# Optimization experiments

Measured on AMD Instinct MI355X. Metric: run time of the kernel, lower is better.

## Reference

```python
import jax, jax.numpy as jnp
import numpy as np
import math

D_MODEL = 512
N_HEADS = 8
D_FF = 2048
E_LAYERS = 2
ENC_IN = 3
MA_K = 25            # moving_avg kernel size
FACTOR = 1
B, L_CYC, CDL = 16, 20, 128
SEQ = L_CYC * CDL    # 2560
TOP_K = int(FACTOR * math.log(SEQ))  # 7
OUTPUT_NUM = 1


def moving_avg(x, k=MA_K):
    # x: [B,S,D]; replicate-pad ends by (k-1)//2, stride-1 mean pool -> length S
    p = (k - 1) // 2
    xp = jnp.concatenate([jnp.repeat(x[:, :1], p, axis=1), x, jnp.repeat(x[:, -1:], p, axis=1)], axis=1)
    c = jnp.cumsum(xp, axis=1)
    c = jnp.concatenate([jnp.zeros_like(c[:, :1]), c], axis=1)
    return (c[:, k:] - c[:, :-k]) / k


def token_embed(x, W):
    # x: [B,S,C], W: [D_MODEL, C, 3]; Conv1d k=3, circular padding, no bias
    xc = jnp.pad(x.transpose(0, 2, 1), ((0, 0), (0, 0), (1, 1)), mode='wrap')
    y = jax.lax.conv_general_dilated(xc, W, (1,), 'VALID', dimension_numbers=('NCH', 'OIH', 'NCH'))
    return y.transpose(0, 2, 1)  # [B,S,D]


def autocorrelation(q, k, v):
    # q,k,v: [B,S,H,E]; FFT autocorrelation + top-k time-delay aggregation (inference path)
    B_, S, H, E = q.shape
    qf = jnp.fft.rfft(q.transpose(0, 2, 3, 1), axis=-1)      # [B,H,E,F]
    kf = jnp.fft.rfft(k.transpose(0, 2, 3, 1), axis=-1)
    corr = jnp.fft.irfft(qf * jnp.conj(kf), n=S, axis=-1)    # [B,H,E,S]
    vals = v.transpose(0, 2, 3, 1)                           # [B,H,E,S]
    mean_corr = corr.mean(axis=(1, 2))                       # [B,S]
    weights, delay = jax.lax.top_k(mean_corr, TOP_K)         # [B,K]
    w = jax.nn.softmax(weights, axis=-1)

    def agg_one(v_b, d_b, w_b):
        # roll by -delay == gather values at index (t + delay) mod S
        out = jnp.zeros_like(v_b)
        for i in range(TOP_K):
            out = out + jnp.roll(v_b, -d_b[i], axis=-1) * w_b[i]
        return out

    V = jax.vmap(agg_one)(vals, delay, w)                    # [B,H,E,S]
    return V.transpose(0, 3, 1, 2)                           # [B,S,H,E]


def my_layernorm(x, g, b):
    # LayerNorm over last dim, then subtract the per-series (time) mean
    mu = x.mean(-1, keepdims=True)
    var = ((x - mu) ** 2).mean(-1, keepdims=True)
    xh = (x - mu) / jnp.sqrt(var + 1e-5) * g + b
    return xh - xh.mean(axis=1, keepdims=True)


def encoder_layer(x, Wq, bq, Wk, bk, Wv, bv, Wo, bo, Wc1, Wc2):
    B_, S, D = x.shape
    H, E = N_HEADS, D // N_HEADS
    q = (x @ Wq + bq).reshape(B_, S, H, E)
    k = (x @ Wk + bk).reshape(B_, S, H, E)
    v = (x @ Wv + bv).reshape(B_, S, H, E)
    att = autocorrelation(q, k, v).reshape(B_, S, D)
    x = x + (att @ Wo + bo)
    x = x - moving_avg(x)                                    # series_decomp1: residual part
    y = jax.nn.gelu(x @ Wc1, approximate=False) @ Wc2        # 1x1 convs, no bias
    z = x + y
    return z - moving_avg(z)                                 # series_decomp2


def setup_inputs() -> dict:
    key = jax.random.key(0)
    ks = jax.random.split(key, 12)
    s = 0.02
    rn = lambda k, shape: jax.random.normal(k, shape, dtype=jnp.float32) * s
    return {
        'cycle_curve_data': jax.random.normal(ks[0], (B, L_CYC, ENC_IN, CDL), dtype=jnp.float32),
        'curve_attn_mask': jnp.ones((B, L_CYC), dtype=jnp.float32),
        'W_emb': rn(ks[1], (D_MODEL, ENC_IN, 3)),
        'Wq': rn(ks[2], (E_LAYERS, D_MODEL, D_MODEL)),
        'bq': jnp.zeros((E_LAYERS, D_MODEL), jnp.float32),
        'Wk': rn(ks[3], (E_LAYERS, D_MODEL, D_MODEL)),
        'bk': jnp.zeros((E_LAYERS, D_MODEL), jnp.float32),
        'Wv': rn(ks[4], (E_LAYERS, D_MODEL, D_MODEL)),
        'bv': jnp.zeros((E_LAYERS, D_MODEL), jnp.float32),
        'Wo': rn(ks[5], (E_LAYERS, D_MODEL, D_MODEL)),
        'bo': jnp.zeros((E_LAYERS, D_MODEL), jnp.float32),
        'Wc1': rn(ks[6], (E_LAYERS, D_MODEL, D_FF)),
        'Wc2': rn(ks[7], (E_LAYERS, D_FF, D_MODEL)),
        'gamma': jnp.ones((D_MODEL,), jnp.float32),
        'beta': jnp.zeros((D_MODEL,), jnp.float32),
        'Wp': rn(ks[8], (D_MODEL * SEQ, OUTPUT_NUM)),
        'bp': jnp.zeros((OUTPUT_NUM,), jnp.float32),
    }


def reference(cycle_curve_data, curve_attn_mask, W_emb, Wq, bq, Wk, bk, Wv, bv, Wo, bo, Wc1, Wc2, gamma, beta, Wp, bp):
    mask = curve_attn_mask[:, :, None, None]                 # [B,L,1,1]
    x = jnp.where(mask == 0, 0.0, cycle_curve_data)          # zero masked cycles
    Bn = x.shape[0]
    x = x.transpose(0, 1, 3, 2).reshape(Bn, SEQ, ENC_IN)     # [B, L*CDL, NV]
    h = token_embed(x, W_emb)                                # DataEmbedding_wo_pos (x_mark=None, dropout=0)
    for l in range(E_LAYERS):
        h = encoder_layer(h, Wq[l], bq[l], Wk[l], bk[l], Wv[l], bv[l], Wo[l], bo[l], Wc1[l], Wc2[l])
    h = my_layernorm(h, gamma, beta)
    out = jax.nn.gelu(h, approximate=False)
    emb = out.reshape(Bn, -1)
    return emb @ Wp + bp                                     # [B, OUTPUT_NUM]
```

## Files before the change

kernel.cpp:

```cpp
#include <hip/hip_runtime.h>
#include <math.h>

#define BATCH 16
#define L_CYC 20
#define CDL 128
#define SEQ 2560
#define ENC_IN 3
#define DMODEL 512
#define DFF 2048
#define NLAYERS 2
#define TOPK 7
#define MROWS (BATCH*SEQ)
#define SD ((size_t)BATCH * SEQ * DMODEL)
#define FFN_CHUNK 20480
#define CHUNK_D 256
#define DGRP 8
#define FFT_NT 512

typedef short bf16x8 __attribute__((ext_vector_type(8)));
typedef float f32x4 __attribute__((ext_vector_type(4)));

__device__ __forceinline__ float gelu_f(float x) {
    return 0.5f * x * (1.0f + erff(x * 0.70710678118654752f));
}
__device__ __forceinline__ unsigned short f2bf(float f) {
    unsigned int u = __float_as_uint(f);
    u += 0x7fff + ((u >> 16) & 1);
    return (unsigned short)(u >> 16);
}
__device__ __forceinline__ float bf2f(unsigned short h) {
    return __uint_as_float(((unsigned int)h) << 16);
}
__device__ __forceinline__ void xcd_map(int p, int G, int& g, int& n) {
    int a = p >> 3;
    n = a % G;
    g = (a / G) * 8 + (p & 7);
}
__device__ __forceinline__ void gload16(const unsigned short* g, unsigned short* l) {
    typedef unsigned int u32;
    __builtin_amdgcn_global_load_lds(
        (const __attribute__((address_space(1))) u32*)g,
        (__attribute__((address_space(3))) u32*)l, 16, 0, 0);
}

__global__ __launch_bounds__(256) void embed_kernel(
    const float* __restrict__ data, const float* __restrict__ mask,
    const float* __restrict__ Wemb, float* __restrict__ h) {
    __shared__ float xv[9];
    size_t idx = (size_t)blockIdx.x * 256 + threadIdx.x;
    size_t r = idx >> 9;
    int s = (int)(r % SEQ);
    int b = (int)(r / SEQ);
    int tid = threadIdx.x;
    if (tid < 9) {
        int t = tid / 3, c = tid % 3;
        int u = s - 1 + t;
        if (u < 0) u += SEQ;
        if (u >= SEQ) u -= SEQ;
        int cyc = u >> 7, pos = u & 127;
        float mk = mask[b * L_CYC + cyc];
        xv[c * 3 + t] = (mk == 0.f) ? 0.f
            : data[(((size_t)b * L_CYC + cyc) * ENC_IN + c) * CDL + pos];
    }
    __syncthreads();
    int dm = idx & (DMODEL - 1);
    float acc = 0.f;
#pragma unroll
    for (int j = 0; j < 9; j++) acc += xv[j] * Wemb[dm * 9 + j];
    h[idx] = acc;
}

__global__ void conv_split_kernel(const float* __restrict__ in,
                                  unsigned short* __restrict__ hi,
                                  unsigned short* __restrict__ lo, size_t n) {
    size_t i = ((size_t)blockIdx.x * 256 + threadIdx.x) * 4;
    if (i >= n) return;
    float4 v = *(const float4*)(in + i);
    float vv[4] = { v.x, v.y, v.z, v.w };
#pragma unroll
    for (int j = 0; j < 4; j++) {
        unsigned short h = f2bf(vv[j]);
        hi[i + j] = h;
        lo[i + j] = f2bf(vv[j] - bf2f(h));
    }
}

__global__ __launch_bounds__(256) void transpose_bf16_kernel(
    const float* __restrict__ W, unsigned short* __restrict__ Wt, int K, int N) {
    __shared__ float t[32][33];
    int n0 = blockIdx.x * 32, k0 = blockIdx.y * 32;
    int c = threadIdx.x & 31, r = threadIdx.x >> 5;
    for (int i = 0; i < 4; i++)
        t[r + i * 8][c] = W[(size_t)(k0 + r + i * 8) * N + n0 + c];
    __syncthreads();
    for (int i = 0; i < 4; i++)
        Wt[(size_t)(n0 + r + i * 8) * K + k0 + c] = f2bf(t[c][r + i * 8]);
}

__global__ __launch_bounds__(256) void transpose_split_stk_kernel(
    const float* __restrict__ W, unsigned short* __restrict__ WtH,
    unsigned short* __restrict__ WtL, int which) {
    __shared__ float t[32][33];
    int n0 = blockIdx.x * 32, k0 = blockIdx.y * 32;
    int c = threadIdx.x & 31, r = threadIdx.x >> 5;
    for (int i = 0; i < 4; i++)
        t[r + i * 8][c] = W[(size_t)(k0 + r + i * 8) * DMODEL + n0 + c];
    __syncthreads();
    for (int i = 0; i < 4; i++) {
        int n = n0 + r + i * 8;
        int row = (n & 255) + ((n >> 8) * 512) + which * 256;
        float v = t[c][r + i * 8];
        unsigned short h = f2bf(v);
        size_t o = (size_t)row * DMODEL + k0 + c;
        WtH[o] = h;
        WtL[o] = f2bf(v - bf2f(h));
    }
}

__global__ void stack_bias_kernel(const float* __restrict__ bq,
                                  const float* __restrict__ bk, float* __restrict__ bstk) {
    int i = blockIdx.x * 256 + threadIdx.x;
    if (i >= 1024) return;
    int c = i >> 9, j = i & 511;
    bstk[i] = (j < 256) ? bq[c * 256 + j] : bk[c * 256 + (j - 256)];
}

__global__ __launch_bounds__(256) void wvo_kernel(
    const float* __restrict__ Wv, const float* __restrict__ Wo,
    float* __restrict__ Wvo) {
    __shared__ float row[DMODEL];
    int k = blockIdx.x;
    int tid = threadIdx.x;
    for (int j = tid; j < DMODEL; j += 256) row[j] = Wv[(size_t)k * DMODEL + j];
    __syncthreads();
    float a0 = 0.f, a1 = 0.f;
    for (int j = 0; j < DMODEL; j++) {
        float wv = row[j];
        a0 += wv * Wo[(size_t)j * DMODEL + tid];
        a1 += wv * Wo[(size_t)j * DMODEL + tid + 256];
    }
    Wvo[(size_t)k * DMODEL + tid] = a0;
    Wvo[(size_t)k * DMODEL + tid + 256] = a1;
}

__global__ void cbias_kernel(const float* __restrict__ bv, const float* __restrict__ Wo,
                             const float* __restrict__ bo, float* __restrict__ cb) {
    int n = blockIdx.x * 256 + threadIdx.x;
    if (n >= DMODEL) return;
    float acc = bo[n];
    for (int j = 0; j < DMODEL; j++) acc += bv[j] * Wo[(size_t)j * DMODEL + n];
    cb[n] = acc;
}

#define BK 32
__global__ __launch_bounds__(256) void gemm_mfma_kernel(
    const unsigned short* __restrict__ A, const unsigned short* __restrict__ Wt,
    const float* __restrict__ bias, const float* res,
    void* Cout, int M, int N, int K, int act, int outMode, int gridN)
{
    __shared__ unsigned short As[128 * 32];
    __shared__ unsigned short Bs[128 * 32];
    int tid = threadIdx.x;
    int wave = tid >> 6, lane = tid & 63;
    int wm = wave & 1, wn = wave >> 1;
    int gblk, nblk;
    xcd_map(blockIdx.x, gridN, gblk, nblk);
    int bm = gblk * 128, bn = nblk * 128;

    int lrs = lane >> 2;
    int lk  = (lane & 3) * 8;

    f32x4 acc[4][4] = {};
    int frow = lane & 15, fk = (lane >> 4) * 8;

    for (int k0 = 0; k0 < K; k0 += BK) {
        __syncthreads();
#pragma unroll
        for (int i = 0; i < 2; i++) {
            int j = wave * 2 + i;
            int row = j * 16 + lrs;
            gload16(A  + (size_t)(bm + row) * K + k0 + lk, As + j * 512);
            gload16(Wt + (size_t)(bn + row) * K + k0 + lk, Bs + j * 512);
        }
        asm volatile("s_waitcnt vmcnt(0)" ::: "memory");
        __syncthreads();
        bf16x8 af[4], bfv[4];
#pragma unroll
        for (int mi = 0; mi < 4; mi++)
            af[mi] = *(const bf16x8*)&As[(wm * 64 + mi * 16 + frow) * 32 + fk];
#pragma unroll
        for (int nj = 0; nj < 4; nj++)
            bfv[nj] = *(const bf16x8*)&Bs[(wn * 64 + nj * 16 + frow) * 32 + fk];
#pragma unroll
        for (int mi = 0; mi < 4; mi++)
#pragma unroll
            for (int nj = 0; nj < 4; nj++)
                acc[mi][nj] = __builtin_amdgcn_mfma_f32_16x16x32_bf16(
                    af[mi], bfv[nj], acc[mi][nj], 0, 0, 0);
    }

    int lrow = (lane >> 4) * 4, lcol = lane & 15;
#pragma unroll
    for (int mi = 0; mi < 4; mi++) {
        int row0 = bm + wm * 64 + mi * 16 + lrow;
#pragma unroll
        for (int nj = 0; nj < 4; nj++) {
            int col = bn + wn * 64 + nj * 16 + lcol;
            float bv = bias ? bias[col] : 0.f;
            f32x4 v = acc[mi][nj];
#pragma unroll
            for (int r = 0; r < 4; r++) {
                int row = row0 + r;
                float x = v[r] + bv;
                if (res) x += res[(size_t)row * N + col];
                if (act == 1) x = gelu_f(x);
                if (outMode == 0) ((float*)Cout)[(size_t)row * N + col] = x;
                else              ((unsigned short*)Cout)[(size_t)row * N + col] = f2bf(x);
            }
        }
    }
}

__global__ __launch_bounds__(256) void gemm_qk_split_kernel(
    const unsigned short* __restrict__ Ahi, const unsigned short* __restrict__ Alo,
    const unsigned short* __restrict__ Whi, const unsigned short* __restrict__ Wlo,
    const float* __restrict__ bias, float* __restrict__ Ct, int M, int K, int gridN)
{
    __shared__ unsigned short AsH[128 * 32];
    __shared__ unsigned short AsL[128 * 32];
    __shared__ unsigned short BsH[128 * 32];
    __shared__ unsigned short BsL[128 * 32];
    int tid = threadIdx.x;
    int wave = tid >> 6, lane = tid & 63;
    int wm = wave & 1, wn = wave >> 1;
    int gblk, nblk;
    xcd_map(blockIdx.x, gridN, gblk, nblk);
    int bm = gblk * 128, bn = nblk * 128;

    int lrs = lane >> 2;
    int lk  = (lane & 3) * 8;

    f32x4 acc[4][4] = {};
    int frow = lane & 15, fk = (lane >> 4) * 8;

    for (int k0 = 0; k0 < K; k0 += BK) {
        __syncthreads();
#pragma unroll
        for (int i = 0; i < 2; i++) {
            int j = wave * 2 + i;
            int row = j * 16 + lrs;
            size_t oa = (size_t)(bm + row) * K + k0 + lk;
            size_t ob = (size_t)(bn + row) * K + k0 + lk;
            gload16(Ahi + oa, AsH + j * 512);
            gload16(Alo + oa, AsL + j * 512);
            gload16(Whi + ob, BsH + j * 512);
            gload16(Wlo + ob, BsL + j * 512);
        }
        asm volatile("s_waitcnt vmcnt(0)" ::: "memory");
        __syncthreads();
        bf16x8 afh[4], afl[4], bfh[4], bfl[4];
#pragma unroll
        for (int mi = 0; mi < 4; mi++) {
            int o = (wm * 64 + mi * 16 + frow) * 32 + fk;
            afh[mi] = *(const bf16x8*)&AsH[o];
            afl[mi] = *(const bf16x8*)&AsL[o];
        }
#pragma unroll
        for (int nj = 0; nj < 4; nj++) {
            int o = (wn * 64 + nj * 16 + frow) * 32 + fk;
            bfh[nj] = *(const bf16x8*)&BsH[o];
            bfl[nj] = *(const bf16x8*)&BsL[o];
        }
#pragma unroll
        for (int mi = 0; mi < 4; mi++)
#pragma unroll
            for (int nj = 0; nj < 4; nj++) {
                acc[mi][nj] = __builtin_amdgcn_mfma_f32_16x16x32_bf16(
                    afh[mi], bfh[nj], acc[mi][nj], 0, 0, 0);
                acc[mi][nj] = __builtin_amdgcn_mfma_f32_16x16x32_bf16(
                    afh[mi], bfl[nj], acc[mi][nj], 0, 0, 0);
                acc[mi][nj] = __builtin_amdgcn_mfma_f32_16x16x32_bf16(
                    afl[mi], bfh[nj], acc[mi][nj], 0, 0, 0);
            }
    }

    int lrow = (lane >> 4) * 4, lcol = lane & 15;
#pragma unroll
    for (int mi = 0; mi < 4; mi++) {
        int row0 = bm + wm * 64 + mi * 16 + lrow;
#pragma unroll
        for (int nj = 0; nj < 4; nj++) {
            int col = bn + wn * 64 + nj * 16 + lcol;
            float bv = bias ? bias[col] : 0.f;
            f32x4 v = acc[mi][nj];
#pragma unroll
            for (int r = 0; r < 4; r++)
                Ct[(size_t)col * M + row0 + r] = v[r] + bv;
        }
    }
}

__device__ __forceinline__ int swz(int a) { return a ^ ((a >> 4) & 15); }

template<int LOGS, int NT>
__device__ __forceinline__ void radix4_stage(const float2* __restrict__ X,
                                             float2* __restrict__ Y,
                                             const float2* __restrict__ w512x,
                                             int tid) {
    const int s = 1 << LOGS;
    for (int t = tid; t < 640; t += NT) {
        int sub = t >> 7, r = t & 127;
        int base = sub << 9;
        int q = r & (s - 1);
        int ps = r - q;
        float2 x0 = X[swz(base + r)];
        float2 x1 = X[swz(base + r + 128)];
        float2 x2 = X[swz(base + r + 256)];
        float2 x3 = X[swz(base + r + 384)];
        float A0r = x0.x + x2.x, A0i = x0.y + x2.y;
        float B0r = x1.x + x3.x, B0i = x1.y + x3.y;
        float A1r = x0.x - x2.x, A1i = x0.y - x2.y;
        float B1r = x1.x - x3.x, B1i = x1.y - x3.y;
        float2 w1 = w512x[ps];
        float w2r = w1.x * w1.x - w1.y * w1.y;
        float w2i = 2.0f * w1.x * w1.y;
        float w3r = w2r * w1.x - w2i * w1.y;
        float w3i = w2r * w1.y + w2i * w1.x;
        float u1r = A1r + B1i, u1i = A1i - B1r;
        float u2r = A0r - B0r, u2i = A0i - B0i;
        float u3r = A1r - B1i, u3i = A1i + B1r;
        int ob = base + q + 4 * ps;
        Y[swz(ob)]         = make_float2(A0r + B0r, A0i + B0i);
        Y[swz(ob + s)]     = make_float2(u1r * w1.x - u1i * w1.y,
                                         u1r * w1.y + u1i * w1.x);
        Y[swz(ob + 2 * s)] = make_float2(u2r * w2r - u2i * w2i,
                                         u2r * w2i + u2i * w2r);
        Y[swz(ob + 3 * s)] = make_float2(u3r * w3r - u3i * w3i,
                                         u3r * w3i + u3i * w3r);
    }
}

template<int NT>
__device__ void fft2560(float2* bufA, float2* bufB, const float2* w512x,
                        const float2* tw, int tid) {
    __syncthreads();
    {
        const float w5r[5] = { 1.f,  0.30901699437494742f, -0.80901699437494742f,
                              -0.80901699437494742f,  0.30901699437494742f };
        const float w5i[5] = { 0.f, -0.95105651629515357f, -0.58778525229247312f,
                               0.58778525229247312f,  0.95105651629515357f };
        float2 x[5];
#pragma unroll
        for (int n1 = 0; n1 < 5; n1++) x[n1] = bufA[swz(n1 * 512 + tid)];
#pragma unroll
        for (int k1 = 0; k1 < 5; k1++) {
            float ar = 0.f, ai = 0.f;
#pragma unroll
            for (int n1 = 0; n1 < 5; n1++) {
                int m = (n1 * k1) % 5;
                ar += x[n1].x * w5r[m] - x[n1].y * w5i[m];
                ai += x[n1].x * w5i[m] + x[n1].y * w5r[m];
            }
            if (k1 == 0) {
                bufB[swz(tid)] = make_float2(ar, ai);
            } else {
                float2 w = tw[k1 - 1];
                bufB[swz(k1 * 512 + tid)] =
                    make_float2(ar * w.x - ai * w.y, ar * w.y + ai * w.x);
            }
        }
    }
    __syncthreads();
    radix4_stage<0, NT>(bufB, bufA, w512x, tid); __syncthreads();
    radix4_stage<2, NT>(bufA, bufB, w512x, tid); __syncthreads();
    radix4_stage<4, NT>(bufB, bufA, w512x, tid); __syncthreads();
    radix4_stage<6, NT>(bufA, bufB, w512x, tid); __syncthreads();
    for (int t = tid; t < 1280; t += NT) {
        int sub = t >> 8, q = t & 255;
        int base = sub << 9;
        float2 a = bufB[swz(base + q)];
        float2 b = bufB[swz(base + q + 256)];
        bufA[swz(base + q)]       = make_float2(a.x + b.x, a.y + b.y);
        bufA[swz(base + q + 256)] = make_float2(a.x - b.x, a.y - b.y);
    }
    __syncthreads();
}

__global__ __launch_bounds__(FFT_NT) void fft_fwd_kernel(
    const float* __restrict__ qt, const float* __restrict__ kt, float* __restrict__ Z)
{
    __shared__ float2 bufA[SEQ];
    __shared__ float2 bufB[SEQ];
    __shared__ float2 w512x[512];
    int d0 = blockIdx.x * DGRP;
    int b = blockIdx.y;
    int tid = threadIdx.x;
    {
        float sn, cs;
        sincosf(-6.283185307179586f * (float)tid / 512.0f, &sn, &cs);
        w512x[tid] = make_float2(cs, sn);
    }
    float2 tw[4];
#pragma unroll
    for (int k1 = 1; k1 <= 4; k1++) {
        float sn, cs;
        sincosf(-2.4543692606170259e-3f * (float)(k1 * tid), &sn, &cs);
        tw[k1 - 1] = make_float2(cs, sn);
    }
    float accR[5], accI[5];
#pragma unroll
    for (int j = 0; j < 5; j++) { accR[j] = 0.f; accI[j] = 0.f; }

    for (int col = 0; col < DGRP; col++) {
        const float* qcol = qt + (size_t)(d0 + col) * MROWS + (size_t)b * SEQ;
        const float* kcol = kt + (size_t)(d0 + col) * MROWS + (size_t)b * SEQ;
        __syncthreads();
        for (int i = tid; i < SEQ; i += FFT_NT)
            bufA[swz(i)] = make_float2(qcol[i], kcol[i]);
        fft2560<FFT_NT>(bufA, bufB, w512x, tw, tid);
#pragma unroll
        for (int j = 0; j < 5; j++) {
            int f = tid + FFT_NT * j;
            int fpos = (f % 5) * 512 + (f / 5);
            int g = f ? (SEQ - f) : 0;
            int gpos = (g % 5) * 512 + (g / 5);
            float2 Z1 = bufA[swz(fpos)], Z2 = bufA[swz(gpos)];
            accR[j] += 0.5f * (Z1.x * Z2.y + Z1.y * Z2.x);
            accI[j] += 0.25f * ((Z1.x * Z1.x + Z1.y * Z1.y)
                              - (Z2.x * Z2.x + Z2.y * Z2.y));
        }
    }
#pragma unroll
    for (int j = 0; j < 5; j++) {
        int f = tid + FFT_NT * j;
        int fpos = (f % 5) * 512 + (f / 5);
        atomicAdd(&Z[((size_t)b * SEQ + fpos) * 2 + 0], accR[j]);
        atomicAdd(&Z[((size_t)b * SEQ + fpos) * 2 + 1], accI[j]);
    }
}

__global__ __launch_bounds__(FFT_NT) void fft_inv_kernel(
    const float* __restrict__ Z, float* __restrict__ mc)
{
    __shared__ float2 bufA[SEQ];
    __shared__ float2 bufB[SEQ];
    __shared__ float2 w512x[512];
    int b = blockIdx.x;
    int tid = threadIdx.x;
    {
        float sn, cs;
        sincosf(-6.283185307179586f * (float)tid / 512.0f, &sn, &cs);
        w512x[tid] = make_float2(cs, sn);
    }
    float2 tw[4];
#pragma unroll
    for (int k1 = 1; k1 <= 4; k1++) {
        float sn, cs;
        sincosf(-2.4543692606170259e-3f * (float)(k1 * tid), &sn, &cs);
        tw[k1 - 1] = make_float2(cs, sn);
    }
    for (int i = tid; i < SEQ; i += FFT_NT) {
        int k1 = i % 5, k2 = i / 5;
        float zr = Z[((size_t)b * SEQ + k1 * 512 + k2) * 2 + 0];
        float zi = Z[((size_t)b * SEQ + k1 * 512 + k2) * 2 + 1];
        bufA[swz(i)] = make_float2(zr, -zi);
    }
    fft2560<FFT_NT>(bufA, bufB, w512x, tw, tid);
    const float scale = 1.0f / (2560.0f * 512.0f);
    for (int j = tid; j < SEQ; j += FFT_NT) {
        int k1 = j >> 9, k2 = j & 511;
        mc[(size_t)b * SEQ + k1 + 5 * k2] = bufA[swz(j)].x * scale;
    }
}

__global__ __launch_bounds__(256) void topk_kernel(
    const float* __restrict__ mc, float* __restrict__ wts, int* __restrict__ dels)
{
    __shared__ float cv[SEQ];
    __shared__ float rv[256];
    __shared__ int   ri[256];
    __shared__ float topv[TOPK];
    __shared__ int   topi[TOPK];
    int b = blockIdx.x, tid = threadIdx.x;
    for (int i = tid; i < SEQ; i += 256) cv[i] = mc[(size_t)b * SEQ + i];
    __syncthreads();
    for (int it = 0; it < TOPK; it++) {
        float bv = -2e30f; int bi = 1 << 30;
        for (int i = tid; i < SEQ; i += 256) {
            float v = cv[i];
            if (v > bv || (v == bv && i < bi)) { bv = v; bi = i; }
        }
        rv[tid] = bv; ri[tid] = bi;
        __syncthreads();
        for (int off = 128; off > 0; off >>= 1) {
            if (tid < off) {
                float v2 = rv[tid + off]; int i2 = ri[tid + off];
                if (v2 > rv[tid] || (v2 == rv[tid] && i2 < ri[tid])) {
                    rv[tid] = v2; ri[tid] = i2;
                }
            }
            __syncthreads();
        }
        if (tid == 0) { topv[it] = rv[0]; topi[it] = ri[0]; cv[ri[0]] = -1e30f; }
        __syncthreads();
    }
    if (tid == 0) {
        float mx = topv[0];
        float e[TOPK], ssum = 0.f;
        for (int i = 0; i < TOPK; i++) { e[i] = expf(topv[i] - mx); ssum += e[i]; }
        for (int i = 0; i < TOPK; i++) {
            wts[b * TOPK + i] = e[i] / ssum;
            dels[b * TOPK + i] = topi[i];
        }
    }
}

__global__ void agg_res_kernel(const float* __restrict__ u, const float* __restrict__ x,
                               const float* __restrict__ cb,
                               const float* __restrict__ wts, const int* __restrict__ dels,
                               float* __restrict__ x1) {
    size_t idx = (size_t)blockIdx.x * 256 + threadIdx.x;
    if (idx >= SD) return;
    int d = idx & (DMODEL - 1);
    size_t r = idx >> 9;
    int s = (int)(r % SEQ);
    int b = (int)(r / SEQ);
    float acc = cb[d] + x[idx];
    for (int i = 0; i < TOPK; i++) {
        int del = dels[b * TOPK + i];
        float w = wts[b * TOPK + i];
        int ss = s + del; if (ss >= SEQ) ss -= SEQ;
        acc += w * u[((size_t)b * SEQ + ss) * DMODEL + d];
    }
    x1[idx] = acc;
}

#define MA_MODE_PLAIN 0
#define MA_MODE_BF    1
#define MA_MODE_SPLIT 2
template<int MODE>
__device__ __forceinline__ void ma_run_body(
    const float* __restrict__ x, float* __restrict__ out,
    unsigned short* __restrict__ o1, unsigned short* __restrict__ o2)
{
    int tid = threadIdx.x;
    int s0 = blockIdx.x * 128;
    int d  = blockIdx.y * 256 + tid;
    int b  = blockIdx.z;
    const float* xb = x + (size_t)b * SEQ * DMODEL + d;
    float sum = 0.f;
#pragma unroll
    for (int j = -12; j <= 12; j++) {
        int ss = s0 + j;
        ss = ss < 0 ? 0 : (ss > SEQ - 1 ? SEQ - 1 : ss);
        sum += xb[(size_t)ss * DMODEL];
    }
    for (int s = s0; s < s0 + 128; s++) {
        float v = xb[(size_t)s * DMODEL] - sum * (1.0f / 25.0f);
        size_t o = ((size_t)b * SEQ + s) * DMODEL + d;
        out[o] = v;
        if (MODE == MA_MODE_BF) {
            o1[o] = f2bf(v);
        } else if (MODE == MA_MODE_SPLIT) {
            unsigned short h = f2bf(v);
            o1[o] = h;
            o2[o] = f2bf(v - bf2f(h));
        }
        int add = s + 13; if (add > SEQ - 1) add = SEQ - 1;
        int sub = s - 12; if (sub < 0) sub = 0;
        sum += xb[(size_t)add * DMODEL] - xb[(size_t)sub * DMODEL];
    }
}
__global__ __launch_bounds__(256) void ma_sub_kernel(
    const float* __restrict__ x, float* __restrict__ out) {
    ma_run_body<MA_MODE_PLAIN>(x, out, nullptr, nullptr);
}
__global__ __launch_bounds__(256) void ma_sub_bf_kernel(
    const float* __restrict__ x, float* __restrict__ out,
    unsigned short* __restrict__ obf) {
    ma_run_body<MA_MODE_BF>(x, out, obf, nullptr);
}
__global__ __launch_bounds__(256) void ma_sub_split_kernel(
    const float* __restrict__ x, float* __restrict__ out,
    unsigned short* __restrict__ hi, unsigned short* __restrict__ lo) {
    ma_run_body<MA_MODE_SPLIT>(x, out, hi, lo);
}

__global__ __launch_bounds__(256) void ln_kernel(
    const float* __restrict__ x, const float* __restrict__ g,
    const float* __restrict__ be, float* __restrict__ xh)
{
    int row = blockIdx.x;
    int tid = threadIdx.x;
    __shared__ float red[256];
    const float* xr = x + (size_t)row * DMODEL;
    float v0 = xr[tid], v1 = xr[tid + 256];
    red[tid] = v0 + v1;
    __syncthreads();
    for (int off = 128; off > 0; off >>= 1) {
        if (tid < off) red[tid] += red[tid + off];
        __syncthreads();
    }
    float mu = red[0] / (float)DMODEL;
    __syncthreads();
    float d0 = v0 - mu, d1 = v1 - mu;
    red[tid] = d0 * d0 + d1 * d1;
    __syncthreads();
    for (int off = 128; off > 0; off >>= 1) {
        if (tid < off) red[tid] += red[tid + off];
        __syncthreads();
    }
    float inv = rsqrtf(red[0] / (float)DMODEL + 1e-5f);
    xh[(size_t)row * DMODEL + tid]       = d0 * inv * g[tid] + be[tid];
    xh[(size_t)row * DMODEL + tid + 256] = d1 * inv * g[tid + 256] + be[tid + 256];
}

__global__ __launch_bounds__(256) void colmean_kernel(
    const float* __restrict__ xh, float* __restrict__ cm) {
    int idx = blockIdx.x * 256 + threadIdx.x;
    int d = idx & (DMODEL - 1), b = idx >> 9;
    int s0 = blockIdx.y * 128;
    float acc = 0.f;
    for (int s = s0; s < s0 + 128; s++)
        acc += xh[((size_t)b * SEQ + s) * DMODEL + d];
    atomicAdd(&cm[idx], acc * (1.0f / (float)SEQ));
}

__global__ __launch_bounds__(256) void final_kernel(
    const float* __restrict__ xh, const float* __restrict__ cm,
    const float* __restrict__ Wp, const float* __restrict__ bp,
    float* __restrict__ out)
{
    int b = blockIdx.y, chunk = blockIdx.x;
    int tid = threadIdx.x;
    const size_t per = (size_t)SEQ * DMODEL / 64;
    size_t start = (size_t)chunk * per;
    float acc = 0.f;
    for (size_t i = start + tid; i < start + per; i += 256) {
        int d = (int)(i & (DMODEL - 1));
        float v = xh[(size_t)b * SEQ * DMODEL + i] - cm[b * DMODEL + d];
        acc += gelu_f(v) * Wp[i];
    }
    __shared__ float red[256];
    red[tid] = acc;
    __syncthreads();
    for (int off = 128; off > 0; off >>= 1) {
        if (tid < off) red[tid] += red[tid + off];
        __syncthreads();
    }
    if (tid == 0) {
        atomicAdd(&out[b], red[0]);
        if (chunk == 0) atomicAdd(&out[b], bp[0]);
    }
}

extern "C" void kernel_launch(void* const* d_in, const int* in_sizes, int n_in,
                              void* d_out, int out_size, void* d_ws, size_t ws_size,
                              hipStream_t stream) {
    const float* data  = (const float*)d_in[0];
    const float* mask  = (const float*)d_in[1];
    const float* Wemb  = (const float*)d_in[2];
    const float* Wq    = (const float*)d_in[3];
    const float* bq    = (const float*)d_in[4];
    const float* Wk    = (const float*)d_in[5];
    const float* bk    = (const float*)d_in[6];
    const float* Wv    = (const float*)d_in[7];
    const float* bv    = (const float*)d_in[8];
    const float* Wo    = (const float*)d_in[9];
    const float* bo    = (const float*)d_in[10];
    const float* Wc1   = (const float*)d_in[11];
    const float* Wc2   = (const float*)d_in[12];
    const float* gamma = (const float*)d_in[13];
    const float* beta  = (const float*)d_in[14];
    const float* Wp    = (const float*)d_in[15];
    const float* bp    = (const float*)d_in[16];
    float* out = (float*)d_out;

    float* buf0 = (float*)d_ws;
    float* buf1 = buf0 + SD;
    float* buf2 = buf1 + SD;

    unsigned short* WstkH = (unsigned short*)(buf2 + SD);
    unsigned short* WstkL = WstkH + 2 * DMODEL * DMODEL;
    unsigned short* Wvot  = WstkL + 2 * DMODEL * DMODEL;
    unsigned short* Wc1t  = Wvot + DMODEL * DMODEL;
    unsigned short* Wc2t  = Wc1t + (size_t)DMODEL * DFF;
    float* WvoF = (float*)(Wc2t + (size_t)DMODEL * DFF);
    float* CB   = WvoF + (size_t)DMODEL * DMODEL;
    float* Bstk = CB + DMODEL;
    float* Zb = Bstk + 1024;
    float* MC = Zb + (size_t)BATCH * SEQ * 2;
    float* WT = MC + (size_t)BATCH * SEQ;
    int*   DL = (int*)(WT + BATCH * TOPK);
    float* CM = (float*)(DL + BATCH * TOPK);

    const int NB  = (int)((SD + 255) / 256);
    const int NB4 = (int)((SD / 4 + 255) / 256);
    dim3 gMA(SEQ / 128, 2, BATCH);

    float* X  = buf0;
    float* HL = buf1;
    float* S  = buf2;

    embed_kernel<<<NB, 256, 0, stream>>>(data, mask, Wemb, X);
    conv_split_kernel<<<NB4, 256, 0, stream>>>(
        X, (unsigned short*)HL + SD, (unsigned short*)HL, SD);

    const int gSqBlocks = (MROWS / 128) * (DMODEL / 128);
    const int gF1Blocks = (FFN_CHUNK / 128) * (DFF / 128);
    const int gF2Blocks = (FFN_CHUNK / 128) * (DMODEL / 128);

    for (int l = 0; l < NLAYERS; l++) {
        const float* wq = Wq + (size_t)l * DMODEL * DMODEL;
        const float* wk = Wk + (size_t)l * DMODEL * DMODEL;
        const float* wv = Wv + (size_t)l * DMODEL * DMODEL;
        const float* wo = Wo + (size_t)l * DMODEL * DMODEL;
        const float* bqL = bq + (size_t)l * DMODEL;
        const float* bkL = bk + (size_t)l * DMODEL;
        const float* bvL = bv + (size_t)l * DMODEL;
        const float* boL = bo + (size_t)l * DMODEL;
        const float* wc1 = Wc1 + (size_t)l * DMODEL * DFF;
        const float* wc2 = Wc2 + (size_t)l * DFF * DMODEL;

        unsigned short* Lbf = (unsigned short*)HL;
        unsigned short* Hbf = Lbf + SD;
        float* qtf = S;
        float* ktf = S + (size_t)MROWS * CHUNK_D;

        dim3 gT(DMODEL / 32, DMODEL / 32);
        transpose_split_stk_kernel<<<gT, 256, 0, stream>>>(wq, WstkH, WstkL, 0);
        transpose_split_stk_kernel<<<gT, 256, 0, stream>>>(wk, WstkH, WstkL, 1);
        stack_bias_kernel<<<4, 256, 0, stream>>>(bqL, bkL, Bstk);
        wvo_kernel<<<DMODEL, 256, 0, stream>>>(wv, wo, WvoF);
        transpose_bf16_kernel<<<gT, 256, 0, stream>>>(WvoF, Wvot, DMODEL, DMODEL);
        cbias_kernel<<<2, 256, 0, stream>>>(bvL, wo, boL, CB);
        transpose_bf16_kernel<<<dim3(DFF / 32, DMODEL / 32), 256, 0, stream>>>(wc1, Wc1t, DMODEL, DFF);
        transpose_bf16_kernel<<<dim3(DMODEL / 32, DFF / 32), 256, 0, stream>>>(wc2, Wc2t, DFF, DMODEL);

        hipMemsetAsync(Zb, 0, (size_t)BATCH * SEQ * 2 * sizeof(float), stream);
        for (int c = 0; c < DMODEL / CHUNK_D; c++) {
            gemm_qk_split_kernel<<<gSqBlocks, 256, 0, stream>>>(
                Hbf, Lbf, WstkH + (size_t)c * 512 * DMODEL,
                WstkL + (size_t)c * 512 * DMODEL, Bstk + c * 512,
                S, MROWS, DMODEL, DMODEL / 128);
            fft_fwd_kernel<<<dim3(CHUNK_D / DGRP, BATCH), FFT_NT, 0, stream>>>(qtf, ktf, Zb);
        }
        fft_inv_kernel<<<BATCH, FFT_NT, 0, stream>>>(Zb, MC);
        topk_kernel<<<BATCH, 256, 0, stream>>>(MC, WT, DL);

        gemm_mfma_kernel<<<gSqBlocks, 256, 0, stream>>>(Hbf, Wvot, nullptr, nullptr, S,
                                                        MROWS, DMODEL, DMODEL, 0, 0,
                                                        DMODEL / 128);
        agg_res_kernel<<<NB, 256, 0, stream>>>(S, X, CB, WT, DL, HL);
        ma_sub_bf_kernel<<<gMA, 256, 0, stream>>>(HL, X, (unsigned short*)S);
        for (int c = 0; c < MROWS / FFN_CHUNK; c++) {
            const unsigned short* x2c = (unsigned short*)S + (size_t)c * FFN_CHUNK * DMODEL;
            float* xz = X + (size_t)c * FFN_CHUNK * DMODEL;
            gemm_mfma_kernel<<<gF1Blocks, 256, 0, stream>>>(x2c, Wc1t, nullptr, nullptr,
                                                            (unsigned short*)HL,
                                                            FFN_CHUNK, DFF, DMODEL, 1, 1,
                                                            DFF / 128);
            gemm_mfma_kernel<<<gF2Blocks, 256, 0, stream>>>((unsigned short*)HL, Wc2t,
                                                            nullptr, xz, xz,
                                                            FFN_CHUNK, DMODEL, DFF, 0, 0,
                                                            DMODEL / 128);
        }
        if (l + 1 < NLAYERS)
            ma_sub_split_kernel<<<gMA, 256, 0, stream>>>(
                X, S, (unsigned short*)HL + SD, (unsigned short*)HL);
        else
            ma_sub_kernel<<<gMA, 256, 0, stream>>>(X, S);
        float* tmp = X; X = S; S = tmp;
    }

    ln_kernel<<<MROWS, 256, 0, stream>>>(X, gamma, beta, HL);
    hipMemsetAsync(CM, 0, (size_t)BATCH * DMODEL * sizeof(float), stream);
    colmean_kernel<<<dim3(32, 20), 256, 0, stream>>>(HL, CM);
    hipMemsetAsync(out, 0, (size_t)out_size * sizeof(float), stream);
    final_kernel<<<dim3(64, BATCH), 256, 0, stream>>>(HL, CM, Wp, bp, out);
}
```

Baseline: 2.189 ms.

## Double-buffer LDS tiles in MFMA GEMMs and use fast erf approximation in GELU

```diff
diff --git a/kernel.cpp b/kernel.cpp
--- a/kernel.cpp
+++ b/kernel.cpp
@@ -21,7 +21,15 @@
 typedef float f32x4 __attribute__((ext_vector_type(4)));
 
 __device__ __forceinline__ float gelu_f(float x) {
-    return 0.5f * x * (1.0f + erff(x * 0.70710678118654752f));
+    float z = x * 0.70710678118654752f;
+    float az = fabsf(z);
+    float t = __builtin_amdgcn_rcpf(1.0f + 0.3275911f * az);
+    float poly = t * (0.254829592f + t * (-0.284496736f + t * (1.421413741f
+               + t * (-1.453152027f + t * 1.061405429f))));
+    float e = __expf(-az * az);
+    float erfv = 1.0f - poly * e;
+    erfv = copysignf(erfv, z);
+    return 0.5f * x * (1.0f + erfv);
 }
 __device__ __forceinline__ unsigned short f2bf(float f) {
     unsigned int u = __float_as_uint(f);
@@ -158,8 +166,8 @@
     const float* __restrict__ bias, const float* res,
     void* Cout, int M, int N, int K, int act, int outMode, int gridN)
 {
-    __shared__ unsigned short As[128 * 32];
-    __shared__ unsigned short Bs[128 * 32];
+    __shared__ unsigned short As[2][128 * 32];
+    __shared__ unsigned short Bs[2][128 * 32];
     int tid = threadIdx.x;
     int wave = tid >> 6, lane = tid & 63;
     int wm = wave & 1, wn = wave >> 1;
@@ -169,34 +177,49 @@
 
     int lrs = lane >> 2;
     int lk  = (lane & 3) * 8;
+    int j0 = wave * 2, j1 = wave * 2 + 1;
+    const unsigned short* Ag0 = A  + (size_t)(bm + j0 * 16 + lrs) * K + lk;
+    const unsigned short* Ag1 = A  + (size_t)(bm + j1 * 16 + lrs) * K + lk;
+    const unsigned short* Bg0 = Wt + (size_t)(bn + j0 * 16 + lrs) * K + lk;
+    const unsigned short* Bg1 = Wt + (size_t)(bn + j1 * 16 + lrs) * K + lk;
 
     f32x4 acc[4][4] = {};
     int frow = lane & 15, fk = (lane >> 4) * 8;
-
-    for (int k0 = 0; k0 < K; k0 += BK) {
-        __syncthreads();
-#pragma unroll
-        for (int i = 0; i < 2; i++) {
-            int j = wave * 2 + i;
-            int row = j * 16 + lrs;
-            gload16(A  + (size_t)(bm + row) * K + k0 + lk, As + j * 512);
-            gload16(Wt + (size_t)(bn + row) * K + k0 + lk, Bs + j * 512);
-        }
-        asm volatile("s_waitcnt vmcnt(0)" ::: "memory");
-        __syncthreads();
+    int nst = K / BK;
+
+    gload16(Ag0, As[0] + j0 * 512);
+    gload16(Ag1, As[0] + j1 * 512);
+    gload16(Bg0, Bs[0] + j0 * 512);
+    gload16(Bg1, Bs[0] + j1 * 512);
+    asm volatile("s_waitcnt vmcnt(0)" ::: "memory");
+    __syncthreads();
+
+    int cur = 0;
+    for (int t = 0; t < nst; ++t) {
+        int nxt = cur ^ 1;
+        if (t + 1 < nst) {
+            int k0 = (t + 1) * BK;
+            gload16(Ag0 + k0, As[nxt] + j0 * 512);
+            gload16(Ag1 + k0, As[nxt] + j1 * 512);
+            gload16(Bg0 + k0, Bs[nxt] + j0 * 512);
+            gload16(Bg1 + k0, Bs[nxt] + j1 * 512);
+        }
         bf16x8 af[4], bfv[4];
 #pragma unroll
         for (int mi = 0; mi < 4; mi++)
-            af[mi] = *(const bf16x8*)&As[(wm * 64 + mi * 16 + frow) * 32 + fk];
+            af[mi] = *(const bf16x8*)&As[cur][(wm * 64 + mi * 16 + frow) * 32 + fk];
 #pragma unroll
         for (int nj = 0; nj < 4; nj++)
-            bfv[nj] = *(const bf16x8*)&Bs[(wn * 64 + nj * 16 + frow) * 32 + fk];
+            bfv[nj] = *(const bf16x8*)&Bs[cur][(wn * 64 + nj * 16 + frow) * 32 + fk];
 #pragma unroll
         for (int mi = 0; mi < 4; mi++)
 #pragma unroll
             for (int nj = 0; nj < 4; nj++)
                 acc[mi][nj] = __builtin_amdgcn_mfma_f32_16x16x32_bf16(
                     af[mi], bfv[nj], acc[mi][nj], 0, 0, 0);
+        asm volatile("s_waitcnt vmcnt(0)" ::: "memory");
+        __syncthreads();
+        cur = nxt;
     }
 
     int lrow = (lane >> 4) * 4, lcol = lane & 15;
@@ -226,10 +249,10 @@
     const unsigned short* __restrict__ Whi, const unsigned short* __restrict__ Wlo,
     const float* __restrict__ bias, float* __restrict__ Ct, int M, int K, int gridN)
 {
-    __shared__ unsigned short AsH[128 * 32];
-    __shared__ unsigned short AsL[128 * 32];
-    __shared__ unsigned short BsH[128 * 32];
-    __shared__ unsigned short BsL[128 * 32];
+    __shared__ unsigned short AsH[2][128 * 32];
+    __shared__ unsigned short AsL[2][128 * 32];
+    __shared__ unsigned short BsH[2][128 * 32];
+    __shared__ unsigned short BsL[2][128 * 32];
     int tid = threadIdx.x;
     int wave = tid >> 6, lane = tid & 63;
     int wm = wave & 1, wn = wave >> 1;
@@ -239,37 +262,53 @@
 
     int lrs = lane >> 2;
     int lk  = (lane & 3) * 8;
+    int j0 = wave * 2, j1 = wave * 2 + 1;
+    size_t oa0 = (size_t)(bm + j0 * 16 + lrs) * K + lk;
+    size_t oa1 = (size_t)(bm + j1 * 16 + lrs) * K + lk;
+    size_t ob0 = (size_t)(bn + j0 * 16 + lrs) * K + lk;
+    size_t ob1 = (size_t)(bn + j1 * 16 + lrs) * K + lk;
 
     f32x4 acc[4][4] = {};
     int frow = lane & 15, fk = (lane >> 4) * 8;
-
-    for (int k0 = 0; k0 < K; k0 += BK) {
-        __syncthreads();
-#pragma unroll
-        for (int i = 0; i < 2; i++) {
-            int j = wave * 2 + i;
-            int row = j * 16 + lrs;
-            size_t oa = (size_t)(bm + row) * K + k0 + lk;
-            size_t ob = (size_t)(bn + row) * K + k0 + lk;
-            gload16(Ahi + oa, AsH + j * 512);
-            gload16(Alo + oa, AsL + j * 512);
-            gload16(Whi + ob, BsH + j * 512);
-            gload16(Wlo + ob, BsL + j * 512);
-        }
-        asm volatile("s_waitcnt vmcnt(0)" ::: "memory");
-        __syncthreads();
+    int nst = K / BK;
+
+    gload16(Ahi + oa0, AsH[0] + j0 * 512);
+    gload16(Ahi + oa1, AsH[0] + j1 * 512);
+    gload16(Alo + oa0, AsL[0] + j0 * 512);
+    gload16(Alo + oa1, AsL[0] + j1 * 512);
+    gload16(Whi + ob0, BsH[0] + j0 * 512);
+    gload16(Whi + ob1, BsH[0] + j1 * 512);
+    gload16(Wlo + ob0, BsL[0] + j0 * 512);
+    gload16(Wlo + ob1, BsL[0] + j1 * 512);
+    asm volatile("s_waitcnt vmcnt(0)" ::: "memory");
+    __syncthreads();
+
+    int cur = 0;
+    for (int t = 0; t < nst; ++t) {
+        int nxt = cur ^ 1;
+        if (t + 1 < nst) {
+            int k0 = (t + 1) * BK;
+            gload16(Ahi + oa0 + k0, AsH[nxt] + j0 * 512);
+            gload16(Ahi + oa1 + k0, AsH[nxt] + j1 * 512);
+            gload16(Alo + oa0 + k0, AsL[nxt] + j0 * 512);
+            gload16(Alo + oa1 + k0, AsL[nxt] + j1 * 512);
+            gload16(Whi + ob0 + k0, BsH[nxt] + j0 * 512);
+            gload16(Whi + ob1 + k0, BsH[nxt] + j1 * 512);
+            gload16(Wlo + ob0 + k0, BsL[nxt] + j0 * 512);
+            gload16(Wlo + ob1 + k0, BsL[nxt] + j1 * 512);
+        }
         bf16x8 afh[4], afl[4], bfh[4], bfl[4];
 #pragma unroll
         for (int mi = 0; mi < 4; mi++) {
             int o = (wm * 64 + mi * 16 + frow) * 32 + fk;
-            afh[mi] = *(const bf16x8*)&AsH[o];
-            afl[mi] = *(const bf16x8*)&AsL[o];
+            afh[mi] = *(const bf16x8*)&AsH[cur][o];
+            afl[mi] = *(const bf16x8*)&AsL[cur][o];
         }
 #pragma unroll
         for (int nj = 0; nj < 4; nj++) {
             int o = (wn * 64 + nj * 16 + frow) * 32 + fk;
-            bfh[nj] = *(const bf16x8*)&BsH[o];
-            bfl[nj] = *(const bf16x8*)&BsL[o];
+            bfh[nj] = *(const bf16x8*)&BsH[cur][o];
+            bfl[nj] = *(const bf16x8*)&BsL[cur][o];
         }
 #pragma unroll
         for (int mi = 0; mi < 4; mi++)
@@ -282,6 +321,9 @@
                 acc[mi][nj] = __builtin_amdgcn_mfma_f32_16x16x32_bf16(
                     afl[mi], bfh[nj], acc[mi][nj], 0, 0, 0);
             }
+        asm volatile("s_waitcnt vmcnt(0)" ::: "memory");
+        __syncthreads();
+        cur = nxt;
     }
 
     int lrow = (lane >> 4) * 4, lcol = lane & 15;
```

New measurement: 2.111 ms. 1.04x faster.
